# Kernel tuning notes

Measured on AMD Instinct MI355X. Metric: run time of the kernel, lower is better.

## Reference

```python
import jax, jax.numpy as jnp
import numpy as np

B, N, D = 8, 512, 3


def setup_inputs() -> dict:
    key = jax.random.key(0)
    ks = jax.random.split(key, 9)
    s = lambda fan_in: 1.0 / np.sqrt(fan_in)
    return {
        "coords": jax.random.normal(ks[0], (B, N, D), jnp.float32),
        "fw0": jax.random.normal(ks[1], (3, 64), jnp.float32) * s(3),
        "fb0": jnp.zeros((64,), jnp.float32),
        "fw1": jax.random.normal(ks[2], (64, 128), jnp.float32) * s(64),
        "fb1": jnp.zeros((128,), jnp.float32),
        "aw0": jax.random.normal(ks[3], (6, 64), jnp.float32) * s(6),
        "ab0": jnp.zeros((64,), jnp.float32),
        "aw1": jax.random.normal(ks[4], (64, 64), jnp.float32) * s(64),
        "ab1": jnp.zeros((64,), jnp.float32),
        "aw2": jax.random.normal(ks[5], (64, 1), jnp.float32) * s(64),
        "ab2": jnp.zeros((1,), jnp.float32),
        "uw0": jax.random.normal(ks[6], (259, 256), jnp.float32) * s(259),
        "ub0": jnp.zeros((256,), jnp.float32),
        "uw1": jax.random.normal(ks[7], (256, 128), jnp.float32) * s(256),
        "ub1": jnp.zeros((128,), jnp.float32),
    }


def reference(coords, fw0, fb0, fw1, fb1, aw0, ab0, aw1, ab1, aw2, ab2,
              uw0, ub0, uw1, ub1):
    relu = jax.nn.relu
    # node feature MLP: (B, N, 3) -> (B, N, 128)
    h = relu(relu(coords @ fw0 + fb0) @ fw1 + fb1)
    # pairwise concat: (B, N, N, 2D)
    nP = coords.shape[1]
    pi = jnp.broadcast_to(coords[:, :, None, :], (B, nP, nP, D))
    pj = jnp.broadcast_to(coords[:, None, :, :], (B, nP, nP, D))
    pair = jnp.concatenate([pi, pj], axis=-1)
    # adjacency MLP -> scalar per pair; note final layer also has relu
    a = relu(pair @ aw0 + ab0)
    a = relu(a @ aw1 + ab1)
    A = relu(a @ aw2 + ab2)[..., 0]  # (B, N, N)
    # aggregate
    V = jnp.matmul(A, h)  # (B, N, 128)
    updates = jnp.concatenate([h, coords, V], axis=-1)  # (B, N, 259)
    h_next = relu(relu(updates @ uw0 + ub0) @ uw1 + ub1)
    # max pool over points
    return jnp.max(h_next, axis=1)  # (B, 128)
```

## Files before the change

kernel.cpp:

```cpp
#include <hip/hip_runtime.h>
#include <hip/hip_bf16.h>

#define B_ 8
#define N_ 512

typedef __attribute__((ext_vector_type(8))) __bf16 bf16x8;
typedef __attribute__((ext_vector_type(8))) _Float16 f16x8;
typedef __attribute__((ext_vector_type(4))) _Float16 f16x4;
typedef __attribute__((ext_vector_type(2))) _Float16 h2;
typedef __attribute__((ext_vector_type(4))) float f32x4;
typedef __attribute__((ext_vector_type(4))) unsigned int u32x4;
typedef __attribute__((ext_vector_type(2))) unsigned int u32x2;

__device__ __forceinline__ unsigned pk_bf16(float hi, float lo) {
    return __builtin_amdgcn_perm(__builtin_bit_cast(unsigned, hi),
                                 __builtin_bit_cast(unsigned, lo), 0x07060302u);
}

__device__ __forceinline__ h2 pkrtz(float a, float b) {
    return __builtin_bit_cast(h2, __builtin_amdgcn_cvt_pkrtz(a, b));
}
__device__ __forceinline__ unsigned pkrtz_u(float a, float b) {
    return __builtin_bit_cast(unsigned, __builtin_amdgcn_cvt_pkrtz(a, b));
}
__device__ __forceinline__ unsigned relu2_u(h2 v) {
    const h2 z2 = {(_Float16)0.0f, (_Float16)0.0f};
    return __builtin_bit_cast(unsigned, __builtin_elementwise_max(v, z2));
}

__global__ __launch_bounds__(256) void k_mega(
    const float* __restrict__ coords,
    const float* __restrict__ fw0, const float* __restrict__ fb0,
    const float* __restrict__ fw1, const float* __restrict__ fb1,
    const float* __restrict__ aw0, const float* __restrict__ ab0,
    const float* __restrict__ aw1, const float* __restrict__ ab1,
    const float* __restrict__ aw2, const float* __restrict__ ab2,
    const float* __restrict__ uw0, const float* __restrict__ uw1,
    __bf16* __restrict__ h_bf, __bf16* __restrict__ h_t,
    __bf16* __restrict__ w0t, __bf16* __restrict__ w1t,
    __bf16* __restrict__ A,
    float* __restrict__ out, int out_size)
{
    const int blk = blockIdx.x;
    const int t = threadIdx.x;

    if (blk < 2048) {
        __shared__ __align__(16) _Float16 s_aw1p[4096];
        __shared__ float s_eb[64];
        __shared__ __align__(8) unsigned s_cj[256][2];

        const int b = blk >> 8;
        const int half = blk & 1;

        {
            const int base = t * 16;
            _Float16 bt[16];
#pragma unroll
            for (int e = 0; e < 16; ++e) {
                int id = base + e;
                int j = id & 7, mm = (id >> 3) & 15, qq = (id >> 7) & 3;
                int ct = (id >> 9) & 3, s = (id >> 11) & 1;
                bt[e] = (_Float16)aw1[(s * 32 + qq * 8 + j) * 64 + ct * 16 + mm];
            }
            *(f16x8*)&s_aw1p[base] = *(f16x8*)&bt[0];
            *(f16x8*)&s_aw1p[base + 8] = *(f16x8*)&bt[8];
            if (t < 64) {
                int qq = t >> 4, ct = (t >> 2) & 3, r = t & 3;
                s_eb[t] = ab1[ct * 16 + qq * 4 + r];
            }
            const float* cj = coords + (size_t)(b * N_ + half * 256 + t) * 3;
            s_cj[t][0] = pkrtz_u(cj[0], cj[1]);
            s_cj[t][1] = pkrtz_u(cj[2], 1.0f);
        }
        __syncthreads();

        const int l = t & 63;
        const int wave = t >> 6;
        const int q = l >> 4;
        const int m = l & 15;
        const int i = (((blk >> 1) & 127) << 2) + wave;

        const float* ci = coords + (size_t)(b * N_ + i) * 3;
        const float ci0 = ci[0], ci1 = ci[1], ci2 = ci[2];

        f16x4 a0f[4];
        {
            const int chb = ((m >> 2) << 3) + (m & 3);
            const int offs[4] = {0, 4, 32, 36};
#pragma unroll
            for (int t4 = 0; t4 < 4; ++t4) {
                const int ch = chb + offs[t4];
                float w3 = aw0[192 + ch], w4 = aw0[256 + ch], w5 = aw0[320 + ch];
                float o = ab0[ch] + ci0 * aw0[ch] + ci1 * aw0[64 + ch]
                                  + ci2 * aw0[128 + ch];
                u32x2 fr;
                fr[0] = (q == 0) ? pkrtz_u(w3, w4) : 0u;
                fr[1] = (q == 0) ? pkrtz_u(w5, o) : 0u;
                a0f[t4] = __builtin_bit_cast(f16x4, fr);
            }
        }

        f16x4 ewf[4];
#pragma unroll
        for (int ct = 0; ct < 4; ++ct) {
            const float* ep = aw2 + ct * 16 + (q << 2);
            u32x2 fr;
            fr[0] = pkrtz_u(ep[0], ep[1]);
            fr[1] = pkrtz_u(ep[2], ep[3]);
            ewf[ct] = __builtin_bit_cast(f16x4, fr);
        }

        f16x8 bfr[2][4];
#pragma unroll
        for (int s = 0; s < 2; ++s)
#pragma unroll
            for (int ct = 0; ct < 4; ++ct)
                bfr[s][ct] = *(const f16x8*)&s_aw1p[s * 2048 + ct * 512 + q * 128 + m * 8];

        f32x4 ab1q[4];
#pragma unroll
        for (int ct = 0; ct < 4; ++ct)
            ab1q[ct] = *(const f32x4*)&s_eb[q * 16 + ct * 4];

        const float ab2s = ab2[0];
        const f32x4 pr0 = {ab2s, ab2s, ab2s, ab2s};
        const f32x4 zf = {0.f, 0.f, 0.f, 0.f};

        __bf16* Arow = A + ((size_t)(b * N_ + i) << 9) + half * 256;

#pragma unroll 1
        for (int tt = 0; tt < 16; ++tt) {
            f16x4 bj = __builtin_bit_cast(f16x4, *(const u32x2*)s_cj[(tt << 4) + m]);

            f32x4 d0 = __builtin_amdgcn_mfma_f32_16x16x16f16(a0f[0], bj, zf, 0, 0, 0);
            f32x4 d1 = __builtin_amdgcn_mfma_f32_16x16x16f16(a0f[1], bj, zf, 0, 0, 0);
            f32x4 d2 = __builtin_amdgcn_mfma_f32_16x16x16f16(a0f[2], bj, zf, 0, 0, 0);
            f32x4 d3 = __builtin_amdgcn_mfma_f32_16x16x16f16(a0f[3], bj, zf, 0, 0, 0);

            u32x4 pa, pb;
            pa[0] = relu2_u(pkrtz(d0[0], d0[1]));
            pa[1] = relu2_u(pkrtz(d0[2], d0[3]));
            pa[2] = relu2_u(pkrtz(d1[0], d1[1]));
            pa[3] = relu2_u(pkrtz(d1[2], d1[3]));
            pb[0] = relu2_u(pkrtz(d2[0], d2[1]));
            pb[1] = relu2_u(pkrtz(d2[2], d2[3]));
            pb[2] = relu2_u(pkrtz(d3[0], d3[1]));
            pb[3] = relu2_u(pkrtz(d3[2], d3[3]));
            f16x8 a0 = __builtin_bit_cast(f16x8, pa);
            f16x8 a1 = __builtin_bit_cast(f16x8, pb);

            f32x4 c0v = __builtin_amdgcn_mfma_f32_16x16x32_f16(bfr[0][0], a0, ab1q[0], 0, 0, 0);
            c0v = __builtin_amdgcn_mfma_f32_16x16x32_f16(bfr[1][0], a1, c0v, 0, 0, 0);
            f32x4 c1v = __builtin_amdgcn_mfma_f32_16x16x32_f16(bfr[0][1], a0, ab1q[1], 0, 0, 0);
            c1v = __builtin_amdgcn_mfma_f32_16x16x32_f16(bfr[1][1], a1, c1v, 0, 0, 0);
            f32x4 c2v = __builtin_amdgcn_mfma_f32_16x16x32_f16(bfr[0][2], a0, ab1q[2], 0, 0, 0);
            c2v = __builtin_amdgcn_mfma_f32_16x16x32_f16(bfr[1][2], a1, c2v, 0, 0, 0);
            f32x4 c3v = __builtin_amdgcn_mfma_f32_16x16x32_f16(bfr[0][3], a0, ab1q[3], 0, 0, 0);
            c3v = __builtin_amdgcn_mfma_f32_16x16x32_f16(bfr[1][3], a1, c3v, 0, 0, 0);

            u32x2 r0, r1, r2, r3;
            r0[0] = relu2_u(pkrtz(c0v[0], c0v[1]));
            r0[1] = relu2_u(pkrtz(c0v[2], c0v[3]));
            r1[0] = relu2_u(pkrtz(c1v[0], c1v[1]));
            r1[1] = relu2_u(pkrtz(c1v[2], c1v[3]));
            r2[0] = relu2_u(pkrtz(c2v[0], c2v[1]));
            r2[1] = relu2_u(pkrtz(c2v[2], c2v[3]));
            r3[0] = relu2_u(pkrtz(c3v[0], c3v[1]));
            r3[1] = relu2_u(pkrtz(c3v[2], c3v[3]));

            f32x4 pr = __builtin_amdgcn_mfma_f32_16x16x16f16(
                ewf[0], __builtin_bit_cast(f16x4, r0), pr0, 0, 0, 0);
            pr = __builtin_amdgcn_mfma_f32_16x16x16f16(
                ewf[1], __builtin_bit_cast(f16x4, r1), pr, 0, 0, 0);
            pr = __builtin_amdgcn_mfma_f32_16x16x16f16(
                ewf[2], __builtin_bit_cast(f16x4, r2), pr, 0, 0, 0);
            pr = __builtin_amdgcn_mfma_f32_16x16x16f16(
                ewf[3], __builtin_bit_cast(f16x4, r3), pr, 0, 0, 0);

            if (l < 16) Arow[(tt << 4) + l] = (__bf16)fmaxf(pr[0], 0.0f);
        }
    } else if (blk < 3072) {
        const int row0 = (blk - 2048) << 2;
        const int b = row0 >> 9;
        const int n0 = row0 & 511;
        __shared__ float cds4[4][4];
        __shared__ float hid4[4][64];
        if (t < 12) {
            int r = t / 3, d = t - 3 * r;
            cds4[r][d] = coords[(size_t)row0 * 3 + t];
        }
        __syncthreads();
        {
            int r = t >> 6, ch = t & 63;
            float v = fb0[ch];
            v += cds4[r][0] * fw0[0 * 64 + ch];
            v += cds4[r][1] * fw0[1 * 64 + ch];
            v += cds4[r][2] * fw0[2 * 64 + ch];
            hid4[r][ch] = fmaxf(v, 0.0f);
        }
        __syncthreads();
        {
            int ch = t & 127;
            int rp = (t >> 7) << 1;
            float hv0 = fb1[ch], hv1 = hv0;
#pragma unroll 4
            for (int k = 0; k < 64; ++k) {
                float w = fw1[k * 128 + ch];
                hv0 += hid4[rp][k] * w;
                hv1 += hid4[rp + 1][k] * w;
            }
            hv0 = fmaxf(hv0, 0.0f);
            hv1 = fmaxf(hv1, 0.0f);
            h_bf[((size_t)(row0 + rp) << 7) + ch] = (__bf16)hv0;
            h_bf[((size_t)(row0 + rp + 1) << 7) + ch] = (__bf16)hv1;
            *(unsigned*)(h_t + (size_t)(b * 128 + ch) * 512 + n0 + rp) =
                pk_bf16(hv1, hv0);
        }
    } else if (blk < 3328) {
        int k = blk - 3072;
        int c = t;
        int src = (k < 128) ? k : (k + 3);
        w0t[(size_t)c * 256 + k] = (__bf16)uw0[(size_t)src * 256 + c];
    } else if (blk < 3456) {
        int id = (blk - 3328) * 256 + t;
        int c = id & 127, k = id >> 7;
        w1t[(size_t)c * 256 + k] = (__bf16)uw1[(size_t)k * 128 + c];
    } else {
        int i = (blk - 3456) * 256 + t;
        if (i < out_size) out[i] = 0.0f;
    }
}

__global__ __launch_bounds__(1024) void k_aggupd(
    const __bf16* __restrict__ A, const __bf16* __restrict__ h_t,
    const __bf16* __restrict__ h_bf, const float* __restrict__ coords,
    const float* __restrict__ uw0, const float* __restrict__ ub0,
    const __bf16* __restrict__ w0t, const __bf16* __restrict__ w1t,
    const float* __restrict__ ub1,
    float* __restrict__ out)
{
    const int t = threadIdx.x;
    const int w = t >> 6;
    const int gw = w & 7;
    const int ks = w >> 3;
    const int l = t & 63;
    const int q = l >> 4;
    const int m = l & 15;
    const int row0 = blockIdx.x << 4;
    const int b = row0 >> 9;

    __shared__ __align__(16) __bf16 act[16][264];
    __shared__ __align__(16) __bf16 u1[16][264];
    __shared__ float vp[2][16][128];
    __shared__ float cds[16][4];

    {
        unsigned hv = *(const unsigned*)(h_bf + ((size_t)row0 << 7) + t * 2);
        *(unsigned*)&act[(t * 2) >> 7][(t * 2) & 127] = hv;
    }
    if (t < 48) {
        int r = t / 3, d = t - 3 * r;
        cds[r][d] = coords[(size_t)row0 * 3 + t];
    }

    const __bf16* Ar = A + (size_t)(row0 + m) * 512 + ks * 256 + q * 8;
    const __bf16* hp = h_t + ((size_t)b << 16) + (size_t)(gw * 16 + m) * 512
                       + ks * 256 + q * 8;
    f32x4 acc = {0.f, 0.f, 0.f, 0.f};
#pragma unroll 4
    for (int kt = 0; kt < 8; ++kt) {
        bf16x8 av = *(const bf16x8*)(Ar + kt * 32);
        bf16x8 bv = *(const bf16x8*)(hp + kt * 32);
        acc = __builtin_amdgcn_mfma_f32_16x16x32_bf16(av, bv, acc, 0, 0, 0);
    }
#pragma unroll
    for (int r = 0; r < 4; ++r)
        vp[ks][q * 4 + r][gw * 16 + m] = acc[r];
    __syncthreads();

#pragma unroll
    for (int it = 0; it < 2; ++it) {
        int idx = t + it * 1024;
        int row = idx >> 7, ch = idx & 127;
        act[row][128 + ch] = (__bf16)(vp[0][row][ch] + vp[1][row][ch]);
    }
    __syncthreads();

    bf16x8 af[8];
#pragma unroll
    for (int ch = 0; ch < 8; ++ch)
        af[ch] = *(const bf16x8*)&act[m][q * 8 + 32 * ch];
    {
        const int c = w * 16 + m;
        const float wx = uw0[128 * 256 + c];
        const float wy = uw0[129 * 256 + c];
        const float wz = uw0[130 * 256 + c];
        const float bias = ub0[c];
        f32x4 a1c;
#pragma unroll
        for (int r = 0; r < 4; ++r)
            a1c[r] = bias + cds[q * 4 + r][0] * wx + cds[q * 4 + r][1] * wy
                          + cds[q * 4 + r][2] * wz;
        const __bf16* wp = w0t + (size_t)c * 256 + q * 8;
#pragma unroll
        for (int ch = 0; ch < 8; ++ch) {
            bf16x8 bfr = *(const bf16x8*)(wp + 32 * ch);
            a1c = __builtin_amdgcn_mfma_f32_16x16x32_bf16(af[ch], bfr, a1c, 0, 0, 0);
        }
#pragma unroll
        for (int r = 0; r < 4; ++r)
            u1[q * 4 + r][c] = (__bf16)fmaxf(a1c[r], 0.0f);
    }
    __syncthreads();

    if (w < 8) {
        bf16x8 af2[8];
#pragma unroll
        for (int ch = 0; ch < 8; ++ch)
            af2[ch] = *(const bf16x8*)&u1[m][q * 8 + 32 * ch];
        const int c = w * 16 + m;
        float bias = ub1[c];
        f32x4 a2c = {bias, bias, bias, bias};
        const __bf16* wp = w1t + (size_t)c * 256 + q * 8;
#pragma unroll
        for (int ch = 0; ch < 8; ++ch) {
            bf16x8 bfr = *(const bf16x8*)(wp + 32 * ch);
            a2c = __builtin_amdgcn_mfma_f32_16x16x32_bf16(af2[ch], bfr, a2c, 0, 0, 0);
        }
        float mx = fmaxf(fmaxf(a2c[0], a2c[1]), fmaxf(a2c[2], a2c[3]));
        mx = fmaxf(mx, 0.0f);
        mx = fmaxf(mx, __shfl_xor(mx, 16, 64));
        mx = fmaxf(mx, __shfl_xor(mx, 32, 64));
        if (l < 16)
            atomicMax((int*)(out + ((size_t)b << 7) + c), __float_as_int(mx));
    }
}

extern "C" void kernel_launch(void* const* d_in, const int* in_sizes, int n_in,
                              void* d_out, int out_size, void* d_ws, size_t ws_size,
                              hipStream_t stream)
{
    const float* coords = (const float*)d_in[0];
    const float* fw0 = (const float*)d_in[1];
    const float* fb0 = (const float*)d_in[2];
    const float* fw1 = (const float*)d_in[3];
    const float* fb1 = (const float*)d_in[4];
    const float* aw0 = (const float*)d_in[5];
    const float* ab0 = (const float*)d_in[6];
    const float* aw1 = (const float*)d_in[7];
    const float* ab1 = (const float*)d_in[8];
    const float* aw2 = (const float*)d_in[9];
    const float* ab2 = (const float*)d_in[10];
    const float* uw0 = (const float*)d_in[11];
    const float* ub0 = (const float*)d_in[12];
    const float* uw1 = (const float*)d_in[13];
    const float* ub1 = (const float*)d_in[14];
    float* out = (float*)d_out;

    char* ws = (char*)d_ws;
    __bf16* A    = (__bf16*)(ws);
    __bf16* h_t  = (__bf16*)(ws + (4u << 20));
    __bf16* h_bf = (__bf16*)(ws + (5u << 20));
    __bf16* w0t  = (__bf16*)(ws + (6u << 20));
    __bf16* w1t  = (__bf16*)(ws + (6u << 20) + (128u << 10));

    k_mega<<<3460, 256, 0, stream>>>(coords, fw0, fb0, fw1, fb1,
                                     aw0, ab0, aw1, ab1, aw2, ab2, uw0, uw1,
                                     h_bf, h_t, w0t, w1t, A, out, out_size);
    k_aggupd<<<256, 1024, 0, stream>>>(A, h_t, h_bf, coords, uw0, ub0,
                                       w0t, w1t, ub1, out);
}
```

Baseline: 128.2 us.

## Process full adjacency rows per block and stage MLP weights in shared memory

```diff
diff --git a/kernel.cpp b/kernel.cpp
--- a/kernel.cpp
+++ b/kernel.cpp
@@ -44,33 +44,45 @@
     const int blk = blockIdx.x;
     const int t = threadIdx.x;
 
-    if (blk < 2048) {
+    if (blk < 1024) {
         __shared__ __align__(16) _Float16 s_aw1p[4096];
-        __shared__ float s_eb[64];
-        __shared__ __align__(8) unsigned s_cj[256][2];
-
-        const int b = blk >> 8;
-        const int half = blk & 1;
+        __shared__ __align__(16) float s_w[576];
+        __shared__ __align__(8) unsigned s_cj[512][2];
+
+        const int b = blk >> 7;
 
         {
-            const int base = t * 16;
-            _Float16 bt[16];
-#pragma unroll
-            for (int e = 0; e < 16; ++e) {
-                int id = base + e;
-                int j = id & 7, mm = (id >> 3) & 15, qq = (id >> 7) & 3;
-                int ct = (id >> 9) & 3, s = (id >> 11) & 1;
-                bt[e] = (_Float16)aw1[(s * 32 + qq * 8 + j) * 64 + ct * 16 + mm];
+            f32x4 wv[4];
+#pragma unroll
+            for (int p = 0; p < 4; ++p)
+                wv[p] = *(const f32x4*)(aw1 + t * 16 + p * 4);
+            const int row = t >> 2;
+            const int ct = t & 3;
+            const int s = row >> 5;
+            const int qq = (row >> 3) & 3;
+            const int j = row & 7;
+            const int base = s * 2048 + ct * 512 + qq * 128 + j;
+#pragma unroll
+            for (int e = 0; e < 16; ++e)
+                s_aw1p[base + e * 8] = (_Float16)wv[e >> 2][e & 3];
+
+            if (t < 144) {
+                const int o = t * 4;
+                f32x4 v;
+                if (o < 384)      v = *(const f32x4*)(aw0 + o);
+                else if (o < 448) v = *(const f32x4*)(ab0 + (o - 384));
+                else if (o < 512) v = *(const f32x4*)(aw2 + (o - 448));
+                else              v = *(const f32x4*)(ab1 + (o - 512));
+                *(f32x4*)&s_w[o] = v;
             }
-            *(f16x8*)&s_aw1p[base] = *(f16x8*)&bt[0];
-            *(f16x8*)&s_aw1p[base + 8] = *(f16x8*)&bt[8];
-            if (t < 64) {
-                int qq = t >> 4, ct = (t >> 2) & 3, r = t & 3;
-                s_eb[t] = ab1[ct * 16 + qq * 4 + r];
+
+            const float* cb = coords + (size_t)b * N_ * 3;
+#pragma unroll
+            for (int jj = t; jj < 512; jj += 256) {
+                const float* cj = cb + jj * 3;
+                s_cj[jj][0] = pkrtz_u(cj[0], cj[1]);
+                s_cj[jj][1] = pkrtz_u(cj[2], 1.0f);
             }
-            const float* cj = coords + (size_t)(b * N_ + half * 256 + t) * 3;
-            s_cj[t][0] = pkrtz_u(cj[0], cj[1]);
-            s_cj[t][1] = pkrtz_u(cj[2], 1.0f);
         }
         __syncthreads();
 
@@ -78,7 +90,7 @@
         const int wave = t >> 6;
         const int q = l >> 4;
         const int m = l & 15;
-        const int i = (((blk >> 1) & 127) << 2) + wave;
+        const int i = ((blk & 127) << 2) + wave;
 
         const float* ci = coords + (size_t)(b * N_ + i) * 3;
         const float ci0 = ci[0], ci1 = ci[1], ci2 = ci[2];
@@ -90,9 +102,9 @@
 #pragma unroll
             for (int t4 = 0; t4 < 4; ++t4) {
                 const int ch = chb + offs[t4];
-                float w3 = aw0[192 + ch], w4 = aw0[256 + ch], w5 = aw0[320 + ch];
-                float o = ab0[ch] + ci0 * aw0[ch] + ci1 * aw0[64 + ch]
-                                  + ci2 * aw0[128 + ch];
+                float w3 = s_w[192 + ch], w4 = s_w[256 + ch], w5 = s_w[320 + ch];
+                float o = s_w[384 + ch] + ci0 * s_w[ch] + ci1 * s_w[64 + ch]
+                                        + ci2 * s_w[128 + ch];
                 u32x2 fr;
                 fr[0] = (q == 0) ? pkrtz_u(w3, w4) : 0u;
                 fr[1] = (q == 0) ? pkrtz_u(w5, o) : 0u;
@@ -103,7 +115,7 @@
         f16x4 ewf[4];
 #pragma unroll
         for (int ct = 0; ct < 4; ++ct) {
-            const float* ep = aw2 + ct * 16 + (q << 2);
+            const float* ep = &s_w[448 + ct * 16 + (q << 2)];
             u32x2 fr;
             fr[0] = pkrtz_u(ep[0], ep[1]);
             fr[1] = pkrtz_u(ep[2], ep[3]);
@@ -120,16 +132,16 @@
         f32x4 ab1q[4];
 #pragma unroll
         for (int ct = 0; ct < 4; ++ct)
-            ab1q[ct] = *(const f32x4*)&s_eb[q * 16 + ct * 4];
+            ab1q[ct] = *(const f32x4*)&s_w[512 + ct * 16 + (q << 2)];
 
         const float ab2s = ab2[0];
         const f32x4 pr0 = {ab2s, ab2s, ab2s, ab2s};
         const f32x4 zf = {0.f, 0.f, 0.f, 0.f};
 
-        __bf16* Arow = A + ((size_t)(b * N_ + i) << 9) + half * 256;
-
-#pragma unroll 1
-        for (int tt = 0; tt < 16; ++tt) {
+        __bf16* Arow = A + ((size_t)(b * N_ + i) << 9);
+
+#pragma unroll 2
+        for (int tt = 0; tt < 32; ++tt) {
             f16x4 bj = __builtin_bit_cast(f16x4, *(const u32x2*)s_cj[(tt << 4) + m]);
 
             f32x4 d0 = __builtin_amdgcn_mfma_f32_16x16x16f16(a0f[0], bj, zf, 0, 0, 0);
@@ -168,19 +180,19 @@
             r3[0] = relu2_u(pkrtz(c3v[0], c3v[1]));
             r3[1] = relu2_u(pkrtz(c3v[2], c3v[3]));
 
-            f32x4 pr = __builtin_amdgcn_mfma_f32_16x16x16f16(
+            f32x4 pra = __builtin_amdgcn_mfma_f32_16x16x16f16(
                 ewf[0], __builtin_bit_cast(f16x4, r0), pr0, 0, 0, 0);
-            pr = __builtin_amdgcn_mfma_f32_16x16x16f16(
-                ewf[1], __builtin_bit_cast(f16x4, r1), pr, 0, 0, 0);
-            pr = __builtin_amdgcn_mfma_f32_16x16x16f16(
-                ewf[2], __builtin_bit_cast(f16x4, r2), pr, 0, 0, 0);
-            pr = __builtin_amdgcn_mfma_f32_16x16x16f16(
-                ewf[3], __builtin_bit_cast(f16x4, r3), pr, 0, 0, 0);
-
-            if (l < 16) Arow[(tt << 4) + l] = (__bf16)fmaxf(pr[0], 0.0f);
-        }
-    } else if (blk < 3072) {
-        const int row0 = (blk - 2048) << 2;
+            pra = __builtin_amdgcn_mfma_f32_16x16x16f16(
+                ewf[1], __builtin_bit_cast(f16x4, r1), pra, 0, 0, 0);
+            f32x4 prb = __builtin_amdgcn_mfma_f32_16x16x16f16(
+                ewf[2], __builtin_bit_cast(f16x4, r2), zf, 0, 0, 0);
+            prb = __builtin_amdgcn_mfma_f32_16x16x16f16(
+                ewf[3], __builtin_bit_cast(f16x4, r3), prb, 0, 0, 0);
+
+            if (l < 16) Arow[(tt << 4) + l] = (__bf16)fmaxf(pra[0] + prb[0], 0.0f);
+        }
+    } else if (blk < 2048) {
+        const int row0 = (blk - 1024) << 2;
         const int b = row0 >> 9;
         const int n0 = row0 & 511;
         __shared__ float cds4[4][4];
@@ -216,17 +228,17 @@
             *(unsigned*)(h_t + (size_t)(b * 128 + ch) * 512 + n0 + rp) =
                 pk_bf16(hv1, hv0);
         }
-    } else if (blk < 3328) {
-        int k = blk - 3072;
+    } else if (blk < 2304) {
+        int k = blk - 2048;
         int c = t;
         int src = (k < 128) ? k : (k + 3);
         w0t[(size_t)c * 256 + k] = (__bf16)uw0[(size_t)src * 256 + c];
-    } else if (blk < 3456) {
-        int id = (blk - 3328) * 256 + t;
+    } else if (blk < 2432) {
+        int id = (blk - 2304) * 256 + t;
         int c = id & 127, k = id >> 7;
         w1t[(size_t)c * 256 + k] = (__bf16)uw1[(size_t)k * 128 + c];
     } else {
-        int i = (blk - 3456) * 256 + t;
+        int i = (blk - 2432) * 256 + t;
         if (i < out_size) out[i] = 0.0f;
     }
 }
@@ -364,7 +376,7 @@
     __bf16* w0t  = (__bf16*)(ws + (6u << 20));
     __bf16* w1t  = (__bf16*)(ws + (6u << 20) + (128u << 10));
 
-    k_mega<<<3460, 256, 0, stream>>>(coords, fw0, fb0, fw1, fb1,
+    k_mega<<<2436, 256, 0, stream>>>(coords, fw0, fb0, fw1, fb1,
                                      aw0, ab0, aw1, ab1, aw2, ab2, uw0, uw1,
                                      h_bf, h_t, w0t, w1t, A, out, out_size);
     k_aggupd<<<256, 1024, 0, stream>>>(A, h_t, h_bf, coords, uw0, ub0,
```

Result: no change. 129.7 us (+1.2%).
